# Kernel tuning notes

Hardware: AMD Instinct MI355X
Metric: run time of the kernel (lower is better)

Reference implementation:

```python
import jax, jax.numpy as jnp
import numpy as np
import math
from jax import lax


def _pos_enc(C, T, V, dtype):
    # spatial positional encoding: position = joint index j for every (t, j)
    pos = jnp.tile(jnp.arange(V, dtype=dtype), T)[:, None]            # (T*V, 1)
    div = jnp.exp(jnp.arange(0, C, 2, dtype=dtype) * (-(math.log(10000.0) / C)))
    ang = pos * div                                                   # (T*V, C//2)
    pe = jnp.stack([jnp.sin(ang), jnp.cos(ang)], axis=-1).reshape(T * V, C)
    return pe.reshape(T, V, C).transpose(2, 0, 1)[None]               # (1, C, T, V)


def _sparsemax(z, axis):
    z = jnp.moveaxis(z, axis, -1)
    K = z.shape[-1]
    zs = jnp.flip(jnp.sort(z, axis=-1), axis=-1)                      # descending
    cs = jnp.cumsum(zs, axis=-1)
    k = jnp.arange(1, K + 1, dtype=z.dtype)
    support = (1.0 + k * zs) > cs
    ks = jnp.sum(support, axis=-1, keepdims=True)                     # support size (int)
    tau = (jnp.take_along_axis(cs, ks - 1, axis=-1) - 1.0) / ks.astype(z.dtype)
    out = jnp.maximum(z - tau, 0.0)
    return jnp.moveaxis(out, -1, axis)


def _conv2d(x, w, b, pad_h=0, stride_h=1):
    out = lax.conv_general_dilated(x, w, (stride_h, 1), ((pad_h, pad_h), (0, 0)),
                                   dimension_numbers=('NCHW', 'OIHW', 'NCHW'))
    return out + b.reshape(1, -1, 1, 1)


def _bn(x, g, be, m, v, eps=1e-5):
    inv = g / jnp.sqrt(v + eps)
    return x * inv.reshape(1, -1, 1, 1) + (be - m * inv).reshape(1, -1, 1, 1)


def reference(x, theta, atts, alphas, v_w, v_b, out_w, out_b, out_g, out_be, out_m, out_v,
              ff_w, ff_b, ff_g, ff_be, ff_m, ff_v):
    N, C, T, V = x.shape
    S = theta.shape[1]

    # positional encoding + kernel attention
    y = x + _pos_enc(C, T, V, x.dtype)
    yf = y.transpose(0, 3, 1, 2).reshape(N, V, C * T)                 # (N, V, C*T)
    sq = jnp.sum(yf * yf, axis=-1)
    d2 = sq[:, :, None] + sq[:, None, :] - 2.0 * jnp.einsum('nvd,nud->nvu', yf, yf)
    d2 = jnp.maximum(d2, 0.0)                                         # cdist^2
    dism = d2 / float((C * T) ** 2)                                   # (d / (C*T))^2
    dism = dism / jnp.max(dism)
    kernel_atten = jnp.exp(-jnp.exp(theta) * dism[:, None])           # (N, S, V, V)
    kernel_atten = _sparsemax(kernel_atten, axis=-2)                  # sparsity_alpha == 2
    attention = atts + kernel_atten * alphas                          # is_regularization=True; dropout in eval

    # value mapping (1x1 conv) + subset aggregation
    vx = jnp.einsum('oc,nctv->notv', v_w.reshape(v_w.shape[0], v_w.shape[1]), x) + v_b.reshape(1, -1, 1, 1)
    y = jnp.einsum('nctu,nsuv->nsctv', vx, attention).reshape(N, S * C, T, V)

    # out_nets: temporal conv (k,1) + BN
    pad = (out_w.shape[2] - 1) // 2
    y = _bn(_conv2d(y, out_w, out_b, pad_h=pad), out_g, out_be, out_m, out_v)
    y = jax.nn.leaky_relu(x + y, negative_slope=0.1)                  # downs1 = identity

    # ff_nets: 1x1 conv + BN
    y2 = _bn(_conv2d(y, ff_w, ff_b), ff_g, ff_be, ff_m, ff_v)
    return jax.nn.leaky_relu(x + y2, negative_slope=0.1)              # downs2 = identity


def setup_inputs() -> dict:
    key = jax.random.key(0)
    ks = jax.random.split(key, 8)
    N, C, T, V, S, K = 64, 128, 128, 25, 3, 7
    Cout = 128
    inp = {}
    inp['x'] = jax.random.normal(ks[0], (N, C, T, V), dtype=jnp.float32)
    inp['theta'] = jax.random.normal(ks[1], (1, S, 1, 1), dtype=jnp.float32) * 0.1
    inp['atts'] = jax.random.normal(ks[2], (1, S, V, V), dtype=jnp.float32) * 0.1
    inp['alphas'] = jnp.ones((1, S, 1, 1), dtype=jnp.float32)
    inp['v_w'] = jax.random.normal(ks[3], (C, C, 1, 1), dtype=jnp.float32) * (1.0 / math.sqrt(C))
    inp['v_b'] = jax.random.normal(ks[4], (C,), dtype=jnp.float32) * 0.01
    inp['out_w'] = jax.random.normal(ks[5], (Cout, S * C, K, 1), dtype=jnp.float32) * (1.0 / math.sqrt(S * C * K))
    inp['out_b'] = jax.random.normal(ks[6], (Cout,), dtype=jnp.float32) * 0.01
    inp['out_g'] = jnp.ones((Cout,), dtype=jnp.float32)
    inp['out_be'] = jnp.zeros((Cout,), dtype=jnp.float32)
    inp['out_m'] = jnp.zeros((Cout,), dtype=jnp.float32)
    inp['out_v'] = jnp.ones((Cout,), dtype=jnp.float32)
    inp['ff_w'] = jax.random.normal(ks[7], (Cout, Cout, 1, 1), dtype=jnp.float32) * (1.0 / math.sqrt(Cout))
    inp['ff_b'] = jnp.zeros((Cout,), dtype=jnp.float32)
    inp['ff_g'] = jnp.ones((Cout,), dtype=jnp.float32)
    inp['ff_be'] = jnp.zeros((Cout,), dtype=jnp.float32)
    inp['ff_m'] = jnp.zeros((Cout,), dtype=jnp.float32)
    inp['ff_v'] = jnp.ones((Cout,), dtype=jnp.float32)
    return inp
```

## Files before the change

### kernel.cpp

```cpp
#include <hip/hip_runtime.h>
#include <hip/hip_bf16.h>
#include <math.h>

typedef __attribute__((ext_vector_type(8))) short s16x8;
typedef __attribute__((ext_vector_type(4))) float f32x4;

static __device__ __forceinline__ float bf2f(unsigned short u){
    unsigned int x = ((unsigned int)u) << 16; float f; __builtin_memcpy(&f,&x,4); return f;
}
static __device__ __forceinline__ unsigned short f2bf(float f){
    unsigned int x; __builtin_memcpy(&x,&f,4);
    unsigned int r = (x + 0x7FFFu + ((x>>16)&1u)) >> 16; return (unsigned short)r;
}

static __device__ __forceinline__ void stage16(const void* g, void* l){
    __builtin_amdgcn_global_load_lds((const __attribute__((address_space(1))) unsigned int*)g,
                                     (__attribute__((address_space(3))) unsigned int*)l, 16, 0, 0);
}


__global__ __launch_bounds__(256) void setup_kernel(const float* __restrict__ x,
                            const float* __restrict__ out_w, const float* __restrict__ ff_w,
                            const float* __restrict__ v_w,  const float* __restrict__ v_b,
                            const float* __restrict__ out_b, const float* __restrict__ out_g,
                            const float* __restrict__ out_be, const float* __restrict__ out_m,
                            const float* __restrict__ out_v,
                            const float* __restrict__ ff_b, const float* __restrict__ ff_g,
                            const float* __restrict__ ff_be, const float* __restrict__ ff_m,
                            const float* __restrict__ ff_v,
                            float* __restrict__ consts, unsigned short* __restrict__ ffA,
                            unsigned short* __restrict__ ypad, float* __restrict__ wbpart,
                            float* __restrict__ pebg, float* __restrict__ TPgb,
                            unsigned short* __restrict__ Wr,
                            unsigned short* __restrict__ xbt, unsigned short* __restrict__ xbu,
                            float* __restrict__ G, float* __restrict__ SX)
{
    __shared__ float tile[64][65];
    const int bid = blockIdx.x;
    const int tid = threadIdx.x;

    if (bid < 6400){
        int jb = bid % 50; int cb = (bid/50) & 1; int n = bid/100;
        int lane = tid & 63, wv = tid >> 6;
        size_t xbase = (size_t)n*409600;
        int jn = jb*64 + lane;
        int tt = jn/25, uu = jn - tt*25;
        size_t xbu_lb = (size_t)n*524288 + (size_t)tt*4096 + uu;
        #pragma unroll
        for (int r=wv; r<64; r+=4){
            float v = x[xbase + (size_t)(cb*64+r)*3200 + jb*64 + lane];
            tile[r][lane] = v;
            xbu[xbu_lb + (size_t)(cb*64+r)*32] = f2bf(v);
        }
        __syncthreads();
        #pragma unroll
        for (int j=wv; j<64; j+=4)
            xbt[xbase + (size_t)(jb*64+j)*128 + cb*64 + lane] = f2bf(tile[lane][j]);
        return;
    }

    if (bid < 7296){
        float* owl = &tile[0][0];
        int wb = bid - 6400;
        int o = wb/7, k = wb%7;
        for (int i=tid; i<384; i+=256) owl[i] = out_w[(size_t)(o*384 + i)*7 + k];
        __syncthreads();
        for (int sci=tid; sci<384; sci+=256){
            int s = sci >> 7, ci = sci & 127;
            const float* ow = owl + s*128;
            float acc = 0.f;
            #pragma unroll 8
            for (int c=0; c<128; ++c) acc += ow[c] * v_w[c*128 + ci];
            int kb = (sci>>5)*7 + k, jj = sci & 31;
            Wr[(size_t)o*2688 + kb*32 + jj] = f2bf(acc);
        }
        return;
    }

    const int stride = 2048*256;
    int i0 = (bid-7296)*256 + tid;
    const float KLN = 9.210340371976184f/128.f;
    for (int i=i0; i<40000;  i+=stride) G[i]  = 0.f;
    for (int i=i0; i<204800; i+=stride) SX[i] = 0.f;
    for (int i=i0; i<16384; i+=stride) ffA[i] = f2bf(ff_w[i]);
    for (int i=i0; i<128; i+=stride){
        float inv  = out_g[i]/sqrtf(out_v[i]+1e-5f);
        consts[i]       = inv;
        consts[128+i]   = out_b[i]*inv + out_be[i] - out_m[i]*inv;
        float invf = ff_g[i]/sqrtf(ff_v[i]+1e-5f);
        consts[256+i]   = invf;
        consts[384+i]   = ff_b[i]*invf + ff_be[i] - ff_m[i]*invf;
    }
    for (int i=i0; i<3200; i+=stride){
        int v = i >> 7, c = i & 127;
        float freq = expf(-(float)(c & ~1) * KLN);
        float ang = (float)v * freq;
        pebg[i] = (c & 1) ? cosf(ang) : sinf(ang);
    }
    for (int i=i0; i<625; i+=stride){
        int u = i/25, v = i%25;
        float acc = 0.f;
        for (int c=0; c<128; ++c){
            float freq = expf(-(float)(c & ~1) * KLN);
            float pu = (c & 1) ? cosf((float)u*freq) : sinf((float)u*freq);
            float pv = (c & 1) ? cosf((float)v*freq) : sinf((float)v*freq);
            acc += pu*pv;
        }
        TPgb[i] = 128.f*acc;
    }
    for (int i=i0; i<2688; i+=stride){
        int o = i/21, rem = i%21, s = rem/7, tc = rem%7;
        int kmin = (tc<3) ? (3-tc) : 0;
        int kmax = (tc>3) ? (10-tc) : 7;
        float acc = 0.f;
        for (int c=0; c<128; ++c){
            const float* wp = out_w + (size_t)(o*384 + s*128 + c)*7;
            float vb = v_b[c];
            for (int k=kmin; k<kmax; ++k) acc += wp[k]*vb;
        }
        wbpart[i] = acc;
    }
    for (int i=i0; i<3686400; i+=stride){
        int n2 = i/57600, r2 = i%57600;
        int pp = r2/384, sc = r2%384;
        int ppos = (pp < 75) ? pp : (3200 + pp);
        ypad[(size_t)(n2*3350 + ppos)*384 + sc] = 0;
    }
}

__global__ __launch_bounds__(256) void gram_part(const unsigned short* __restrict__ xbt,
                                                 float* __restrict__ G, float* __restrict__ SX){
    __shared__ float glx[4][32][32];
    int bid = blockIdx.x; int n = bid >> 3; int chunk = bid & 7;
    int tid = threadIdx.x;
    const unsigned short* xb = xbt + (size_t)n*409600;

    int c = tid & 127, th = tid >> 7;
    float a[25];
    #pragma unroll
    for (int u=0; u<25; ++u) a[u] = 0.f;
    for (int tt=0; tt<8; ++tt){
        int t = chunk*16 + th*8 + tt;
        const unsigned short* row = xb + (size_t)t*3200 + c;
        #pragma unroll
        for (int u=0; u<25; ++u) a[u] += bf2f(row[u*128]);
    }
    float* tmp = &glx[0][0][0];
    if (th){
        #pragma unroll
        for (int u=0; u<25; ++u) tmp[u*128+c] = a[u];
    }
    __syncthreads();
    if (!th){
        #pragma unroll
        for (int u=0; u<25; ++u) atomicAdd(&SX[n*3200 + u*128 + c], a[u] + tmp[u*128+c]);
    }
    __syncthreads();

    int lane = tid & 63, w = tid >> 6;
    int lr = lane & 15, lg = lane >> 4;
    f32x4 acc[2][2];
    #pragma unroll
    for (int i2=0;i2<2;i2++)
        #pragma unroll
        for (int j2=0;j2<2;j2++) acc[i2][j2] = (f32x4){0.f,0.f,0.f,0.f};
    for (int tt=0; tt<4; ++tt){
        int t = chunk*16 + w*4 + tt;
        const unsigned short* tb = xb + (size_t)t*3200;
        #pragma unroll
        for (int kc=0; kc<4; ++kc){
            s16x8 f0 = *(const s16x8*)(tb + (size_t)(lr)*128    + kc*32 + lg*8);
            s16x8 f1 = *(const s16x8*)(tb + (size_t)(16+lr)*128 + kc*32 + lg*8);
            acc[0][0] = __builtin_amdgcn_mfma_f32_16x16x32_bf16(f0, f0, acc[0][0], 0,0,0);
            acc[0][1] = __builtin_amdgcn_mfma_f32_16x16x32_bf16(f0, f1, acc[0][1], 0,0,0);
            acc[1][0] = __builtin_amdgcn_mfma_f32_16x16x32_bf16(f1, f0, acc[1][0], 0,0,0);
            acc[1][1] = __builtin_amdgcn_mfma_f32_16x16x32_bf16(f1, f1, acc[1][1], 0,0,0);
        }
    }
    #pragma unroll
    for (int mh=0; mh<2; ++mh)
        #pragma unroll
        for (int nh=0; nh<2; ++nh)
            #pragma unroll
            for (int r=0; r<4; ++r)
                glx[w][mh*16 + lg*4 + r][nh*16 + lr] = acc[mh][nh][r];
    __syncthreads();
    for (int idx=tid; idx<625; idx+=256){
        int u = idx/25, v = idx%25;
        atomicAdd(&G[n*625 + idx], glx[0][u][v] + glx[1][u][v] + glx[2][u][v] + glx[3][u][v]);
    }
}

__global__ __launch_bounds__(256) void gram_fin(const float* __restrict__ SX,
                                                const float* __restrict__ pebg,
                                                const float* __restrict__ TPgb,
                                                float* __restrict__ G){
    __shared__ float sxl[25][129];
    __shared__ float pebl[25][129];
    int n = blockIdx.x, tid = threadIdx.x;
    for (int i=tid; i<3200; i+=256){
        sxl[i>>7][i&127]  = SX[n*3200 + i];
        pebl[i>>7][i&127] = pebg[i];
    }
    __syncthreads();
    for (int idx=tid; idx<625; idx+=256){
        int u = idx/25, v = idx%25;
        float cr = TPgb[idx];
        #pragma unroll 4
        for (int cc=0; cc<128; ++cc)
            cr += sxl[u][cc]*pebl[v][cc] + sxl[v][cc]*pebl[u][cc];
        G[n*625 + idx] += cr;
    }
}

__global__ __launch_bounds__(1024) void attn_kernel(const float* __restrict__ G, const float* __restrict__ theta,
                                                    const float* __restrict__ atts, const float* __restrict__ alphas,
                                                    unsigned short* __restrict__ att_pad, float* __restrict__ asum){
    __shared__ float red[1024];
    int tid = threadIdx.x;
    float mx = 0.f;
    for (int idx=tid; idx<40000; idx+=1024){
        int n = idx/625, r = idx%625, u2 = r/25, v2 = r%25;
        const float* Gn = G + n*625;
        float d2v = fmaxf(Gn[u2*26] + Gn[v2*26] - 2.f*Gn[u2*25+v2], 0.f);
        mx = fmaxf(mx, d2v);
    }
    red[tid] = mx; __syncthreads();
    for (int s2=512; s2>0; s2>>=1){ if (tid < s2) red[tid] = fmaxf(red[tid], red[tid+s2]); __syncthreads(); }
    float inv = 1.f/red[0];
    for (int i=tid; i<64*160; i+=1024){
        int n2 = i/160, r2 = i%160;
        att_pad[n2*2560 + 2400 + r2] = 0;
    }
    for (int col=tid; col<4800; col+=1024){
        int n = col/75, r = col%75, s = r/25, vc = r%25;
        const float* Gn = G + n*625;
        float et = expf(theta[s]);
        float al = alphas[s];
        float gvv = Gn[vc*26];
        float z[25];
        #pragma unroll
        for (int u2=0; u2<25; ++u2){
            float d2v = fmaxf(Gn[u2*26] + gvv - 2.f*Gn[u2*25+vc], 0.f);
            z[u2] = expf(-et*d2v*inv);
        }
        float zm = z[0];
        #pragma unroll
        for (int u2=1; u2<25; ++u2) zm = fmaxf(zm, z[u2]);
        float lo = zm - 1.f, hi = zm;
        for (int it=0; it<30; ++it){
            float mid = 0.5f*(lo+hi);
            float f = 0.f;
            #pragma unroll
            for (int u2=0; u2<25; ++u2) f += fmaxf(z[u2]-mid, 0.f);
            if (f >= 1.f) lo = mid; else hi = mid;
        }
        float ssum = 0.f; int kcnt = 0;
        #pragma unroll
        for (int u2=0; u2<25; ++u2){ if (z[u2] > lo){ ssum += z[u2]; kcnt++; } }
        float tau = (ssum - 1.f)/(float)kcnt;
        float as_ = 0.f;
        unsigned short* apr = att_pad + n*2560 + (s*25+vc)*32;
        #pragma unroll
        for (int u2=0; u2<25; ++u2){
            float av = atts[s*625 + u2*25 + vc] + fmaxf(z[u2]-tau, 0.f)*al;
            apr[u2] = f2bf(av);
            as_ += av;
        }
        #pragma unroll
        for (int u2=25; u2<32; ++u2) apr[u2] = 0;
        asum[n*75 + s*25 + vc] = as_;
    }
}

__global__ __launch_bounds__(256,2) void agg_mfma(const unsigned short* __restrict__ att_pad,
                                                  const unsigned short* __restrict__ xbu,
                                                  unsigned short* __restrict__ ypad){
    int bid = blockIdx.x; int n = bid >> 4; int tb = bid & 15;
    int tid = threadIdx.x; int lane = tid & 63; int w = tid >> 6;
    int lr = lane & 15, lg = lane >> 4;
    const unsigned short* ap = att_pad + n*2560;
    s16x8 a[5];
    #pragma unroll
    for (int mf=0; mf<5; ++mf) a[mf] = *(const s16x8*)&ap[(mf*16+lr)*32 + lg*8];
    int rowoff[5][4];
    #pragma unroll
    for (int mf=0; mf<5; ++mf)
        #pragma unroll
        for (int r=0; r<4; ++r){
            int m = mf*16 + lg*4 + r;
            int s = m/25, v = m - s*25;
            rowoff[mf][r] = (m < 75) ? (v*384 + s*128 + lr) : -1;
        }
    #pragma unroll
    for (int ti=0; ti<2; ++ti){
        int t = tb*8 + w*2 + ti;
        const unsigned short* bp = xbu + (size_t)n*524288 + (size_t)t*4096;
        size_t obase = ((size_t)(n*3350 + 75 + t*25))*384;
        #pragma unroll
        for (int h=0; h<2; ++h){
            s16x8 b[4];
            #pragma unroll
            for (int q=0; q<4; ++q){
                b[q] = *(const s16x8*)&bp[(h*64 + q*16 + lr)*32 + lg*8];
                if (lg == 3){
                    s16x8 t2 = b[q];
                    b[q] = (s16x8){t2[0],0,0,0,0,0,0,0};
                }
            }
            f32x4 acc[5][4];
            #pragma unroll
            for (int mf=0; mf<5; ++mf)
                #pragma unroll
                for (int q=0; q<4; ++q)
                    acc[mf][q] = (f32x4){0.f,0.f,0.f,0.f};
            #pragma unroll
            for (int mf=0; mf<5; ++mf)
                #pragma unroll
                for (int q=0; q<4; ++q)
                    acc[mf][q] = __builtin_amdgcn_mfma_f32_16x16x32_bf16(a[mf], b[q], acc[mf][q], 0, 0, 0);
            #pragma unroll
            for (int mf=0; mf<5; ++mf)
                #pragma unroll
                for (int q=0; q<4; ++q)
                    #pragma unroll
                    for (int r=0; r<4; ++r)
                        if (rowoff[mf][r] >= 0)
                            ypad[obase + rowoff[mf][r] + h*64 + q*16] = f2bf(acc[mf][q][r]);
        }
    }
}

__global__ __launch_bounds__(256,3) void gemm_fused(const unsigned short* __restrict__ Amat,
                                                    const unsigned short* __restrict__ Bsrc,
                                                    const float* __restrict__ xin,
                                                    const float* __restrict__ consts,
                                                    const unsigned short* __restrict__ ffA,
                                                    const float* __restrict__ wbpart,
                                                    const float* __restrict__ asum,
                                                    float* __restrict__ outf)
{
    constexpr int NKB = 42;
    __shared__ unsigned short smem[22936];

    const int tid = threadIdx.x;
    const int bid = blockIdx.x;
    const int n   = bid/25;
    const int jn0 = (bid%25)*128;

    const int lane = tid & 63, wv = tid >> 6;
    const int wm = wv >> 1, wn = wv & 1;
    const int lr = lane & 15, lg = lane >> 4;
    const int swz = (lg ^ (lr&3)) << 3;

    unsigned short* sA = smem;
    unsigned short* sB = smem + 8192;

    auto stage = [&](int kb){
        #pragma unroll
        for (int p=0; p<4; ++p){
            int e = p*256 + tid;
            int r = e >> 3, cch = e & 7;
            int half = cch >> 2, cc = (cch&3) ^ (r&3);
            stage16(Amat + (size_t)r*2688 + kb*64 + half*32 + cc*8, sA + e*8);
        }
        int k32a = 2*kb, k32b = 2*kb + 1;
        int k0 = k32a % 7, s0 = (k32a/7)*32;
        int k1 = k32b % 7, s1 = (k32b/7)*32;
        const unsigned short* b0 = Bsrc + ((size_t)(n*3350 + jn0 + 25*k0))*384 + s0;
        const unsigned short* b1 = Bsrc + ((size_t)(n*3350 + jn0 + 25*k1))*384 + s1;
        #pragma unroll
        for (int p=0; p<4; ++p){
            int e = p*256 + tid;
            int r = e >> 3, cch = e & 7;
            int half = cch >> 2, cc = (cch&3) ^ (r&3);
            const unsigned short* src = (half ? b1 : b0) + (size_t)r*384 + cc*8;
            stage16(src, sB + e*8);
        }
    };

    f32x4 acc[4][4];
    #pragma unroll
    for (int a2=0;a2<4;a2++)
        #pragma unroll
        for (int b2=0;b2<4;b2++) acc[a2][b2] = (f32x4){0.f,0.f,0.f,0.f};

    for (int kb=0; kb<NKB; ++kb){
        stage(kb);
        __syncthreads();
        s16x8 a[4][2], b[4][2];
        #pragma unroll
        for (int mf=0; mf<4; ++mf)
            #pragma unroll
            for (int kf=0; kf<2; ++kf)
                a[mf][kf] = *(const s16x8*)&sA[(wm*64+mf*16+lr)*64 + kf*32 + swz];
        #pragma unroll
        for (int nf=0; nf<4; ++nf)
            #pragma unroll
            for (int kf=0; kf<2; ++kf)
                b[nf][kf] = *(const s16x8*)&sB[(wn*64+nf*16+lr)*64 + kf*32 + swz];
        __builtin_amdgcn_s_setprio(1);
        #pragma unroll
        for (int kf=0; kf<2; ++kf)
            #pragma unroll
            for (int mf=0; mf<4; ++mf)
                #pragma unroll
                for (int nf=0; nf<4; ++nf)
                    acc[mf][nf] = __builtin_amdgcn_mfma_f32_16x16x32_bf16(a[mf][kf], b[nf][kf], acc[mf][nf], 0, 0, 0);
        __builtin_amdgcn_s_setprio(0);
        __syncthreads();
    }

    float* wbl = (float*)(smem + 17408);
    float* asl = wbl + 2688;
    for (int i=tid; i<2688; i+=256) wbl[i] = wbpart[i];
    for (int i=tid; i<75;   i+=256) asl[i] = asum[n*75 + i];
    __syncthreads();

    #pragma unroll
    for (int nf=0; nf<4; ++nf){
        int cj = wn*64 + nf*16 + lr;
        int j  = jn0 + cj;
        int t  = j/25, v = j - t*25;
        int tc = (t<3) ? t : ((t>124) ? (t-121) : 3);
        float a0 = asl[v], a1 = asl[25+v], a2 = asl[50+v];
        #pragma unroll
        for (int mf=0; mf<4; ++mf)
            #pragma unroll
            for (int r=0; r<4; ++r){
                int m = wm*64 + mf*16 + lg*4 + r;
                float b2v = wbl[m*21+tc]*a0 + wbl[m*21+7+tc]*a1 + wbl[m*21+14+tc]*a2;
                float val = acc[mf][nf][r]*consts[m] + consts[128+m] + b2v
                          + xin[(size_t)n*409600 + (size_t)m*3200 + j];
                val = (val >= 0.f) ? val : 0.1f*val;
                smem[cj*136 + m] = f2bf(val);
            }
    }
    __syncthreads();

    f32x4 acc2[4][4];
    #pragma unroll
    for (int a2=0;a2<4;a2++)
        #pragma unroll
        for (int b2=0;b2<4;b2++) acc2[a2][b2] = (f32x4){0.f,0.f,0.f,0.f};
    #pragma unroll
    for (int kb2=0; kb2<4; ++kb2){
        s16x8 a2[4], b2[4];
        #pragma unroll
        for (int mf=0; mf<4; ++mf)
            a2[mf] = *(const s16x8*)&ffA[(size_t)(wm*64+mf*16+lr)*128 + kb2*32 + lg*8];
        #pragma unroll
        for (int nf=0; nf<4; ++nf)
            b2[nf] = *(const s16x8*)&smem[(wn*64+nf*16+lr)*136 + kb2*32 + lg*8];
        #pragma unroll
        for (int mf=0; mf<4; ++mf)
            #pragma unroll
            for (int nf=0; nf<4; ++nf)
                acc2[mf][nf] = __builtin_amdgcn_mfma_f32_16x16x32_bf16(a2[mf], b2[nf], acc2[mf][nf], 0, 0, 0);
    }

    #pragma unroll
    for (int mf=0; mf<4; ++mf)
        #pragma unroll
        for (int r=0; r<4; ++r){
            int co = wm*64 + mf*16 + lg*4 + r;
            float sc2 = consts[256+co], bi2 = consts[384+co];
            #pragma unroll
            for (int nf=0; nf<4; ++nf){
                int cj = wn*64 + nf*16 + lr;
                size_t idx = (size_t)n*409600 + (size_t)co*3200 + jn0 + cj;
                float val = acc2[mf][nf][r]*sc2 + bi2 + xin[idx];
                val = (val >= 0.f) ? val : 0.1f*val;
                outf[idx] = val;
            }
        }
}

extern "C" void kernel_launch(void* const* d_in, const int* in_sizes, int n_in,
                              void* d_out, int out_size, void* d_ws, size_t ws_size,
                              hipStream_t stream) {
    const float* x      = (const float*)d_in[0];
    const float* theta  = (const float*)d_in[1];
    const float* atts   = (const float*)d_in[2];
    const float* alphas = (const float*)d_in[3];
    const float* v_w    = (const float*)d_in[4];
    const float* v_b    = (const float*)d_in[5];
    const float* out_w  = (const float*)d_in[6];
    const float* out_b  = (const float*)d_in[7];
    const float* out_g  = (const float*)d_in[8];
    const float* out_be = (const float*)d_in[9];
    const float* out_m  = (const float*)d_in[10];
    const float* out_v  = (const float*)d_in[11];
    const float* ff_w   = (const float*)d_in[12];
    const float* ff_b   = (const float*)d_in[13];
    const float* ff_g   = (const float*)d_in[14];
    const float* ff_be  = (const float*)d_in[15];
    const float* ff_m   = (const float*)d_in[16];
    const float* ff_v   = (const float*)d_in[17];
    float* out = (float*)d_out;

    char* w = (char*)d_ws;
    size_t off = 0;
    auto alloc = [&](size_t b){ size_t r = off; off += (b + 1023) & ~(size_t)1023; return r; };
    float*          G      = (float*)         (w + alloc(160000));
    float*          SX     = (float*)         (w + alloc(819200));
    float*          asumb  = (float*)         (w + alloc(19200));
    float*          consts = (float*)         (w + alloc(2048));
    float*          wbpart = (float*)         (w + alloc(10752));
    float*          pebg   = (float*)         (w + alloc(12800));
    float*          TPgb   = (float*)         (w + alloc(2500));
    unsigned short* att_pad= (unsigned short*)(w + alloc(327680));
    unsigned short* Wr     = (unsigned short*)(w + alloc(688128));
    unsigned short* ffA    = (unsigned short*)(w + alloc(32768));
    unsigned short* xbt    = (unsigned short*)(w + alloc(52428800 + 16384));
    unsigned short* xbu    = (unsigned short*)(w + alloc(67108864));
    unsigned short* ypad   = (unsigned short*)(w + alloc(164659200));

    setup_kernel<<<9344,256,0,stream>>>(x, out_w, ff_w, v_w, v_b, out_b, out_g, out_be, out_m, out_v,
                                        ff_b, ff_g, ff_be, ff_m, ff_v,
                                        consts, ffA, ypad, wbpart, pebg, TPgb, Wr, xbt, xbu, G, SX);
    gram_part<<<512,256,0,stream>>>(xbt, G, SX);
    gram_fin<<<64,256,0,stream>>>(SX, pebg, TPgb, G);
    attn_kernel<<<1,1024,0,stream>>>(G, theta, atts, alphas, att_pad, asumb);
    agg_mfma<<<1024,256,0,stream>>>(att_pad, xbu, ypad);
    gemm_fused<<<1600,256,0,stream>>>(Wr, ypad, x, consts, ffA, wbpart, asumb, out);
}
```

Measured before the change: 573.6 us.

## Parallelize attention across batch blocks and raise gemm_fused occupancy

The per-sample max of the distance matrix is now computed in gram_fin from a shared-memory copy of G and written to a small buffer. attn_kernel, which ran as a single 1024-thread block, now runs one 128-thread block per sample, reducing the 64 maxima locally and reading G from LDS. Separately, gemm_fused drops its LDS copy of wbpart and reads it from global memory instead, shrinking shared memory so the launch bound can go from 3 to 4 blocks per CU. The cost is redundant global reads of wbpart in the epilogue and extra launch-time work in gram_fin.

```diff
diff --git a/kernel.cpp b/kernel.cpp
--- a/kernel.cpp
+++ b/kernel.cpp
@@ -194,9 +194,12 @@
 __global__ __launch_bounds__(256) void gram_fin(const float* __restrict__ SX,
                                                 const float* __restrict__ pebg,
                                                 const float* __restrict__ TPgb,
-                                                float* __restrict__ G){
+                                                float* __restrict__ G,
+                                                float* __restrict__ nmax){
     __shared__ float sxl[25][129];
     __shared__ float pebl[25][129];
+    __shared__ float gf[625];
+    __shared__ float red[256];
     int n = blockIdx.x, tid = threadIdx.x;
     for (int i=tid; i<3200; i+=256){
         sxl[i>>7][i&127]  = SX[n*3200 + i];
@@ -209,39 +212,49 @@
         #pragma unroll 4
         for (int cc=0; cc<128; ++cc)
             cr += sxl[u][cc]*pebl[v][cc] + sxl[v][cc]*pebl[u][cc];
-        G[n*625 + idx] += cr;
-    }
-}
-
-__global__ __launch_bounds__(1024) void attn_kernel(const float* __restrict__ G, const float* __restrict__ theta,
-                                                    const float* __restrict__ atts, const float* __restrict__ alphas,
-                                                    unsigned short* __restrict__ att_pad, float* __restrict__ asum){
-    __shared__ float red[1024];
-    int tid = threadIdx.x;
+        float val = G[n*625 + idx] + cr;
+        G[n*625 + idx] = val;
+        gf[idx] = val;
+    }
+    __syncthreads();
     float mx = 0.f;
-    for (int idx=tid; idx<40000; idx+=1024){
-        int n = idx/625, r = idx%625, u2 = r/25, v2 = r%25;
-        const float* Gn = G + n*625;
-        float d2v = fmaxf(Gn[u2*26] + Gn[v2*26] - 2.f*Gn[u2*25+v2], 0.f);
-        mx = fmaxf(mx, d2v);
+    for (int idx=tid; idx<625; idx+=256){
+        int u = idx/25, v = idx%25;
+        float d2 = fmaxf(gf[u*26] + gf[v*26] - 2.f*gf[u*25+v], 0.f);
+        mx = fmaxf(mx, d2);
     }
     red[tid] = mx; __syncthreads();
-    for (int s2=512; s2>0; s2>>=1){ if (tid < s2) red[tid] = fmaxf(red[tid], red[tid+s2]); __syncthreads(); }
+    for (int s2=128; s2>0; s2>>=1){ if (tid < s2) red[tid] = fmaxf(red[tid], red[tid+s2]); __syncthreads(); }
+    if (tid == 0) nmax[n] = red[0];
+}
+
+__global__ __launch_bounds__(128) void attn_kernel(const float* __restrict__ G, const float* __restrict__ nmax,
+                                                   const float* __restrict__ theta,
+                                                   const float* __restrict__ atts, const float* __restrict__ alphas,
+                                                   unsigned short* __restrict__ att_pad, float* __restrict__ asum){
+    __shared__ float gl[625];
+    __shared__ float red[64];
+    int n = blockIdx.x, tid = threadIdx.x;
+    if (tid < 64) red[tid] = nmax[tid];
+    for (int i=tid; i<625; i+=128) gl[i] = G[n*625 + i];
+    __syncthreads();
+    if (tid == 0){
+        float m = red[0];
+        for (int i=1; i<64; ++i) m = fmaxf(m, red[i]);
+        red[0] = m;
+    }
+    __syncthreads();
     float inv = 1.f/red[0];
-    for (int i=tid; i<64*160; i+=1024){
-        int n2 = i/160, r2 = i%160;
-        att_pad[n2*2560 + 2400 + r2] = 0;
-    }
-    for (int col=tid; col<4800; col+=1024){
-        int n = col/75, r = col%75, s = r/25, vc = r%25;
-        const float* Gn = G + n*625;
+    for (int i=tid; i<160; i+=128) att_pad[n*2560 + 2400 + i] = 0;
+    if (tid < 75){
+        int s = tid/25, vc = tid%25;
         float et = expf(theta[s]);
         float al = alphas[s];
-        float gvv = Gn[vc*26];
+        float gvv = gl[vc*26];
         float z[25];
         #pragma unroll
         for (int u2=0; u2<25; ++u2){
-            float d2v = fmaxf(Gn[u2*26] + gvv - 2.f*Gn[u2*25+vc], 0.f);
+            float d2v = fmaxf(gl[u2*26] + gvv - 2.f*gl[u2*25+vc], 0.f);
             z[u2] = expf(-et*d2v*inv);
         }
         float zm = z[0];
@@ -331,7 +344,7 @@
     }
 }
 
-__global__ __launch_bounds__(256,3) void gemm_fused(const unsigned short* __restrict__ Amat,
+__global__ __launch_bounds__(256,4) void gemm_fused(const unsigned short* __restrict__ Amat,
                                                     const unsigned short* __restrict__ Bsrc,
                                                     const float* __restrict__ xin,
                                                     const float* __restrict__ consts,
@@ -341,7 +354,7 @@
                                                     float* __restrict__ outf)
 {
     constexpr int NKB = 42;
-    __shared__ unsigned short smem[22936];
+    __shared__ unsigned short smem[17560];
 
     const int tid = threadIdx.x;
     const int bid = blockIdx.x;
@@ -411,10 +424,8 @@
         __syncthreads();
     }
 
-    float* wbl = (float*)(smem + 17408);
-    float* asl = wbl + 2688;
-    for (int i=tid; i<2688; i+=256) wbl[i] = wbpart[i];
-    for (int i=tid; i<75;   i+=256) asl[i] = asum[n*75 + i];
+    float* asl = (float*)(smem + 17408);
+    for (int i=tid; i<75; i+=256) asl[i] = asum[n*75 + i];
     __syncthreads();
 
     #pragma unroll
@@ -429,7 +440,7 @@
             #pragma unroll
             for (int r=0; r<4; ++r){
                 int m = wm*64 + mf*16 + lg*4 + r;
-                float b2v = wbl[m*21+tc]*a0 + wbl[m*21+7+tc]*a1 + wbl[m*21+14+tc]*a2;
+                float b2v = wbpart[m*21+tc]*a0 + wbpart[m*21+7+tc]*a1 + wbpart[m*21+14+tc]*a2;
                 float val = acc[mf][nf][r]*consts[m] + consts[128+m] + b2v
                           + xin[(size_t)n*409600 + (size_t)m*3200 + j];
                 val = (val >= 0.f) ? val : 0.1f*val;
@@ -504,6 +515,7 @@
     auto alloc = [&](size_t b){ size_t r = off; off += (b + 1023) & ~(size_t)1023; return r; };
     float*          G      = (float*)         (w + alloc(160000));
     float*          SX     = (float*)         (w + alloc(819200));
+    float*          nmaxb  = (float*)         (w + alloc(256));
     float*          asumb  = (float*)         (w + alloc(19200));
     float*          consts = (float*)         (w + alloc(2048));
     float*          wbpart = (float*)         (w + alloc(10752));
@@ -520,8 +532,8 @@
                                         ff_b, ff_g, ff_be, ff_m, ff_v,
                                         consts, ffA, ypad, wbpart, pebg, TPgb, Wr, xbt, xbu, G, SX);
     gram_part<<<512,256,0,stream>>>(xbt, G, SX);
-    gram_fin<<<64,256,0,stream>>>(SX, pebg, TPgb, G);
-    attn_kernel<<<1,1024,0,stream>>>(G, theta, atts, alphas, att_pad, asumb);
+    gram_fin<<<64,256,0,stream>>>(SX, pebg, TPgb, G, nmaxb);
+    attn_kernel<<<64,128,0,stream>>>(G, nmaxb, theta, atts, alphas, att_pad, asumb);
     agg_mfma<<<1024,256,0,stream>>>(att_pad, xbu, ypad);
     gemm_fused<<<1600,256,0,stream>>>(Wr, ypad, x, consts, ffA, wbpart, asumb, out);
 }
```

Result: slower. 965.8 us (+68.4%).
